# Kernel optimization log

Hardware: AMD Instinct MI355X
Metric: run time of the kernel (lower is better)

## Reference

```python
import jax, jax.numpy as jnp
import numpy as np
from jax import lax

NUM_GROUPS = 256
GROUP_SIZE = 32
RADIUS = 0.1


def setup_inputs() -> dict:
    key = jax.random.key(0)
    k1, k2 = jax.random.split(key)
    B, N, C = 8, 16384, 128
    # xyz in unit cube so radius=0.1 ball query is meaningful
    p = jax.random.uniform(k1, (B, N, 3), dtype=jnp.float32)
    x = jax.random.normal(k2, (B, C, N), dtype=jnp.float32)
    return {"p": p, "x": x}


def furthest_point_sample(p, m):
    # p: [B,N,3] -> idx [B,m]; standard FPS starting at index 0
    B, N, _ = p.shape

    def step(carry, _):
        dist, last = carry
        cur = jnp.take_along_axis(p, last[:, None, None], axis=1)  # [B,1,3]
        d = jnp.sum((p - cur) ** 2, axis=-1)                        # [B,N]
        dist = jnp.minimum(dist, d)
        nxt = jnp.argmax(dist, axis=1).astype(jnp.int32)
        return (dist, nxt), nxt

    dist0 = jnp.full((B, N), 1e10, dtype=p.dtype)
    idx0 = jnp.zeros((B,), dtype=jnp.int32)
    _, rest = lax.scan(step, (dist0, idx0), None, length=m - 1)  # [m-1,B]
    return jnp.concatenate([idx0[:, None], rest.T], axis=1)      # [B,m]


def ball_query(radius, nsample, support, query):
    # support [B,N,3], query [B,M,3] -> idx [B,M,nsample]
    # CUDA ball_query semantics: first `nsample` points (in index order) within
    # radius; slots past the count are padded with the first found index.
    B, N, _ = support.shape
    d2 = jnp.sum((query[:, :, None, :] - support[:, None, :, :]) ** 2, axis=-1)  # [B,M,N]
    within = d2 < radius * radius
    rng = jnp.arange(N, dtype=jnp.int32)
    keys = jnp.where(within, rng, rng + N)   # in-radius first, preserving index order
    neg_vals, _ = lax.top_k(-keys, nsample)  # nsample smallest keys
    keys_k = -neg_vals                       # [B,M,nsample], ascending
    idx = keys_k % N
    valid = keys_k < N
    return jnp.where(valid, idx, idx[..., :1])  # pad with first neighbor (center itself)


def reference(p, x):
    B, C, N = x.shape
    idx = furthest_point_sample(p, NUM_GROUPS)                              # [B,M] int32
    center_p = jnp.take_along_axis(p, idx[:, :, None].astype(jnp.int32), axis=1)  # [B,M,3]
    center_x = jnp.take_along_axis(x, idx[:, None, :], axis=2)[..., None]   # [B,C,M,1]

    nidx = ball_query(RADIUS, GROUP_SIZE, p, center_p)                      # [B,M,ns]
    bidx = jnp.arange(B)[:, None, None]
    gp = p[bidx, nidx]                                                      # [B,M,ns,3]
    # relative xyz (QueryAndGroup relative_xyz=True, normalize_dp=False)
    grouped_p = gp.transpose(0, 3, 1, 2) - center_p.transpose(0, 2, 1)[:, :, :, None]  # [B,3,M,ns]
    fj = x.transpose(0, 2, 1)[bidx, nidx].transpose(0, 3, 1, 2)             # [B,C,M,ns]
    return grouped_p, center_p, fj, center_x
```

## Files before the change

### kernel.cpp

```cpp
#include <hip/hip_runtime.h>
#include <hip/hip_bf16.h>

#define BB 8
#define NN 16384
#define CC 128
#define MM 256
#define NS 32
#define FPS_T 1024
#define PPT (NN / FPS_T)

#define OFF_GP  0
#define OFF_CP  196608
#define OFF_FJ  202752
#define OFF_CX  8591360

__global__ __launch_bounds__(FPS_T)
__attribute__((amdgpu_waves_per_eu(4, 4)))
void fps_kernel(const float* __restrict__ p, int* __restrict__ idx_out)
{
    __shared__ float s_xy[NN * 2];
    __shared__ unsigned long long s_key[2][16];

    const int b = blockIdx.x;
    const int t = threadIdx.x;
    const int lane = t & 63;
    const float* pb = p + (size_t)b * NN * 3;

    float pz[PPT], dist[PPT];
#pragma unroll
    for (int k = 0; k < PPT; ++k) {
        const int n = t + k * FPS_T;
        s_xy[2 * n + 0] = pb[n * 3 + 0];
        s_xy[2 * n + 1] = pb[n * 3 + 1];
        pz[k] = pb[n * 3 + 2];
        dist[k] = 1e10f;
    }
#pragma unroll
    for (int k = 0; k < PPT; ++k) {
        asm volatile("" : "+v"(pz[k]));
    }

    float cx = pb[0], cy = pb[1], cz = pb[2];
    if (t == 0) idx_out[b * MM + 0] = 0;
    __syncthreads();

    for (int i = 1; i < MM; ++i) {
        float bv = -1.0f;
#pragma unroll
        for (int k = 0; k < PPT; ++k) {
            const int n = t + k * FPS_T;
            const float2 xy = *(const float2*)&s_xy[2 * n];
            const float dx = __fsub_rn(xy.x, cx);
            const float dy = __fsub_rn(xy.y, cy);
            const float dz = __fsub_rn(pz[k], cz);
            const float d = __fadd_rn(
                __fadd_rn(__fmul_rn(dx, dx), __fmul_rn(dy, dy)),
                __fmul_rn(dz, dz));
            const float nd = fminf(dist[k], d);
            dist[k] = nd;
            bv = fmaxf(bv, nd);
        }
        int kb = 0;
#pragma unroll
        for (int k = PPT - 1; k >= 0; --k) {
            if (dist[k] == bv) kb = k;
        }
        const int bn = t + (kb << 10);
        unsigned long long key =
            ((unsigned long long)__float_as_uint(bv) << 32) |
            (unsigned int)(~bn);
#pragma unroll
        for (int off = 32; off > 0; off >>= 1) {
            const unsigned long long ok = __shfl_xor(key, off);
            if (ok > key) key = ok;
        }
        const int buf = i & 1;
        if (lane == 0) s_key[buf][t >> 6] = key;
        __syncthreads();
        unsigned long long fk = s_key[buf][lane & 15];
#pragma unroll
        for (int off = 8; off > 0; off >>= 1) {
            const unsigned long long ok = __shfl_xor(fk, off);
            if (ok > fk) fk = ok;
        }
        const int fn = __builtin_amdgcn_readfirstlane(~((unsigned int)fk));
        cx = pb[fn * 3 + 0];
        cy = pb[fn * 3 + 1];
        cz = pb[fn * 3 + 2];
        if (t == 0) idx_out[b * MM + i] = fn;
    }
}

__global__ __launch_bounds__(64) void ballq_kernel(
    const float* __restrict__ p, const int* __restrict__ idx,
    int* __restrict__ nidx, float* __restrict__ grouped_p,
    float* __restrict__ center_p)
{
    const int bm = blockIdx.x;
    const int b = bm >> 8;
    const int m = bm & 255;
    const int lane = threadIdx.x;
    const float* pb = p + (size_t)b * NN * 3;

    const int cidx = idx[bm];
    const float cx = pb[cidx * 3 + 0];
    const float cy = pb[cidx * 3 + 1];
    const float cz = pb[cidx * 3 + 2];

    if (lane < 3) {
        center_p[bm * 3 + lane] = (lane == 0) ? cx : (lane == 1) ? cy : cz;
    }

    const float R2 = 0.01f;

    __shared__ int lidx[NS];

    int found = 0;
    for (int base = 0; base < NN && found < NS; base += 128) {
        const int n0 = base + lane;
        const int n1 = base + 64 + lane;
        const float dx0 = __fsub_rn(pb[n0 * 3 + 0], cx);
        const float dy0 = __fsub_rn(pb[n0 * 3 + 1], cy);
        const float dz0 = __fsub_rn(pb[n0 * 3 + 2], cz);
        const float d20 = __fadd_rn(
            __fadd_rn(__fmul_rn(dx0, dx0), __fmul_rn(dy0, dy0)),
            __fmul_rn(dz0, dz0));
        const float dx1 = __fsub_rn(pb[n1 * 3 + 0], cx);
        const float dy1 = __fsub_rn(pb[n1 * 3 + 1], cy);
        const float dz1 = __fsub_rn(pb[n1 * 3 + 2], cz);
        const float d21 = __fadd_rn(
            __fadd_rn(__fmul_rn(dx1, dx1), __fmul_rn(dy1, dy1)),
            __fmul_rn(dz1, dz1));
        const bool w0 = d20 < R2;
        const bool w1 = d21 < R2;
        const unsigned long long m0 = __ballot(w0);
        const unsigned long long m1 = __ballot(w1);
        const int pc0 = (int)__popcll(m0);
        const unsigned long long below = (1ull << lane) - 1ull;
        const int slot0 = found + __popcll(m0 & below);
        const int slot1 = found + pc0 + __popcll(m1 & below);
        if (w0 && slot0 < NS) lidx[slot0] = n0;
        if (w1 && slot1 < NS) lidx[slot1] = n1;
        found += pc0 + (int)__popcll(m1);
    }
    __syncthreads();

    const int nfound = found < NS ? found : NS;
    if (lane < NS) {
        const int s = lane;
        const int n = (s < nfound) ? lidx[s] : lidx[0];
        nidx[bm * NS + s] = n;
        const float gx = __fsub_rn(pb[n * 3 + 0], cx);
        const float gy = __fsub_rn(pb[n * 3 + 1], cy);
        const float gz = __fsub_rn(pb[n * 3 + 2], cz);
        grouped_p[(((size_t)b * 3 + 0) * MM + m) * NS + s] = gx;
        grouped_p[(((size_t)b * 3 + 1) * MM + m) * NS + s] = gy;
        grouped_p[(((size_t)b * 3 + 2) * MM + m) * NS + s] = gz;
    }
}

__global__ __launch_bounds__(256) void fj_kernel(
    const float* __restrict__ x, const int* __restrict__ nidx,
    float* __restrict__ fj)
{
    const int bm = blockIdx.x;
    const int b = bm >> 8;
    const int m = bm & 255;

    __shared__ int lidx[NS];
    if (threadIdx.x < NS) lidx[threadIdx.x] = nidx[bm * NS + threadIdx.x];
    __syncthreads();

    const int s  = threadIdx.x & 31;
    const int c0 = threadIdx.x >> 5;
    const int n = lidx[s];
    const float* xb = x + (size_t)b * CC * NN;
    float* ob = fj + (size_t)b * CC * MM * NS + (size_t)m * NS + s;

#pragma unroll
    for (int c = c0; c < CC; c += 8) {
        ob[(size_t)c * MM * NS] = xb[(size_t)c * NN + n];
    }
}

__global__ __launch_bounds__(256) void cx_kernel(
    const float* __restrict__ x, const int* __restrict__ idx,
    float* __restrict__ center_x)
{
    const int bc = blockIdx.x;
    const int b = bc >> 7;
    const int m = threadIdx.x;
    const int n = idx[b * MM + m];
    center_x[(size_t)bc * MM + m] = x[(size_t)bc * NN + n];
}

extern "C" void kernel_launch(void* const* d_in, const int* in_sizes, int n_in,
                              void* d_out, int out_size, void* d_ws, size_t ws_size,
                              hipStream_t stream) {
    const float* p = (const float*)d_in[0];
    const float* x = (const float*)d_in[1];
    float* out = (float*)d_out;

    float* grouped_p = out + OFF_GP;
    float* center_p  = out + OFF_CP;
    float* fj        = out + OFF_FJ;
    float* center_x  = out + OFF_CX;

    int* idx  = (int*)d_ws;
    int* nidx = idx + BB * MM;

    fps_kernel<<<BB, FPS_T, 0, stream>>>(p, idx);
    ballq_kernel<<<BB * MM, 64, 0, stream>>>(p, idx, nidx, grouped_p, center_p);
    fj_kernel<<<BB * MM, 256, 0, stream>>>(x, nidx, fj);
    cx_kernel<<<BB * CC, 256, 0, stream>>>(x, idx, center_x);
}
```

Measured before the change: 686.5 us.

## Split FPS across four blocks per batch with global-memory slot synchronization

Furthest point sampling is spread over 4 workgroups per batch (32 blocks instead of 8), each owning a quarter of the points. Per-iteration argmax keys are exchanged through zeroed global slots with agent-scope atomics and spin-waiting, which replaces the block-level __syncthreads reduction. This cuts the per-iteration distance work per block and uses more CUs, at the cost of a global-memory round trip each iteration. The slot buffer borrows the fj output region, which fj_kernel overwrites later. It relies on all 32 blocks being resident at once, and the spin has a bounded retry count.

Result: slower. 2.664 ms (+288.0%).

```diff
diff --git a/kernel.cpp b/kernel.cpp
--- a/kernel.cpp
+++ b/kernel.cpp
@@ -6,32 +6,47 @@
 #define CC 128
 #define MM 256
 #define NS 32
-#define FPS_T 1024
-#define PPT (NN / FPS_T)
+
+#define NB 4
+#define FT 512
+#define NPB (NN / NB)
+#define PPT (NPB / FT)
+#define WPB 8
+#define SLOTS_PER_ITER (NB * WPB)
+#define SYNC_U64 (BB * MM * SLOTS_PER_ITER)
 
 #define OFF_GP  0
 #define OFF_CP  196608
 #define OFF_FJ  202752
 #define OFF_CX  8591360
 
-__global__ __launch_bounds__(FPS_T)
-__attribute__((amdgpu_waves_per_eu(4, 4)))
-void fps_kernel(const float* __restrict__ p, int* __restrict__ idx_out)
-{
-    __shared__ float s_xy[NN * 2];
-    __shared__ unsigned long long s_key[2][16];
-
-    const int b = blockIdx.x;
-    const int t = threadIdx.x;
+__global__ __launch_bounds__(1024) void zero_kernel(unsigned long long* sync)
+{
+    sync[blockIdx.x * 1024 + threadIdx.x] = 0ull;
+}
+
+__global__ __launch_bounds__(FT) void fps_kernel(
+    const float* __restrict__ p, int* __restrict__ idx_out,
+    unsigned long long* __restrict__ sync)
+{
+    __shared__ float s_xy[NPB * 2];
+
+    const int gb   = blockIdx.x;
+    const int r    = gb >> 2;
+    const int blk  = gb & (NB - 1);
+    const int t    = threadIdx.x;
     const int lane = t & 63;
-    const float* pb = p + (size_t)b * NN * 3;
+    const int w    = t >> 6;
+    const float* pb = p + (size_t)r * NN * 3;
+    const int base = blk * NPB;
 
     float pz[PPT], dist[PPT];
 #pragma unroll
     for (int k = 0; k < PPT; ++k) {
-        const int n = t + k * FPS_T;
-        s_xy[2 * n + 0] = pb[n * 3 + 0];
-        s_xy[2 * n + 1] = pb[n * 3 + 1];
+        const int nl = t + k * FT;
+        const int n  = base + nl;
+        s_xy[2 * nl + 0] = pb[n * 3 + 0];
+        s_xy[2 * nl + 1] = pb[n * 3 + 1];
         pz[k] = pb[n * 3 + 2];
         dist[k] = 1e10f;
     }
@@ -41,15 +56,17 @@
     }
 
     float cx = pb[0], cy = pb[1], cz = pb[2];
-    if (t == 0) idx_out[b * MM + 0] = 0;
+    if (blk == 0 && t == 0) idx_out[r * MM + 0] = 0;
     __syncthreads();
+
+    unsigned long long* slots_b = sync + (size_t)r * MM * SLOTS_PER_ITER;
+    const int myslot = blk * WPB + w;
 
     for (int i = 1; i < MM; ++i) {
         float bv = -1.0f;
 #pragma unroll
         for (int k = 0; k < PPT; ++k) {
-            const int n = t + k * FPS_T;
-            const float2 xy = *(const float2*)&s_xy[2 * n];
+            const float2 xy = *(const float2*)&s_xy[2 * (t + k * FT)];
             const float dx = __fsub_rn(xy.x, cx);
             const float dy = __fsub_rn(xy.y, cy);
             const float dz = __fsub_rn(pz[k], cz);
@@ -65,7 +82,7 @@
         for (int k = PPT - 1; k >= 0; --k) {
             if (dist[k] == bv) kb = k;
         }
-        const int bn = t + (kb << 10);
+        const int bn = base + t + kb * FT;
         unsigned long long key =
             ((unsigned long long)__float_as_uint(bv) << 32) |
             (unsigned int)(~bn);
@@ -74,20 +91,28 @@
             const unsigned long long ok = __shfl_xor(key, off);
             if (ok > key) key = ok;
         }
-        const int buf = i & 1;
-        if (lane == 0) s_key[buf][t >> 6] = key;
-        __syncthreads();
-        unsigned long long fk = s_key[buf][lane & 15];
-#pragma unroll
-        for (int off = 8; off > 0; off >>= 1) {
-            const unsigned long long ok = __shfl_xor(fk, off);
-            if (ok > fk) fk = ok;
-        }
-        const int fn = __builtin_amdgcn_readfirstlane(~((unsigned int)fk));
-        cx = pb[fn * 3 + 0];
-        cy = pb[fn * 3 + 1];
-        cz = pb[fn * 3 + 2];
-        if (t == 0) idx_out[b * MM + i] = fn;
+        unsigned long long* it_slots = slots_b + (size_t)i * SLOTS_PER_ITER;
+        if (lane == 0) {
+            __hip_atomic_store(&it_slots[myslot], key, __ATOMIC_RELEASE,
+                               __HIP_MEMORY_SCOPE_AGENT);
+        }
+        unsigned long long my;
+        int tries = 0;
+        do {
+            my = __hip_atomic_load(&it_slots[lane & 31], __ATOMIC_ACQUIRE,
+                                   __HIP_MEMORY_SCOPE_AGENT);
+        } while (!__all(my != 0ull) && ++tries < 65536);
+#pragma unroll
+        for (int off = 16; off > 0; off >>= 1) {
+            const unsigned long long ok = __shfl_xor(my, off);
+            if (ok > my) my = ok;
+        }
+        const int fn = ~((unsigned int)my);
+        if (blk == 0 && t == 0) idx_out[r * MM + i] = fn;
+        const int fnu = __builtin_amdgcn_readfirstlane(fn);
+        cx = pb[fnu * 3 + 0];
+        cy = pb[fnu * 3 + 1];
+        cz = pb[fnu * 3 + 2];
     }
 }
 
@@ -209,7 +234,10 @@
     int* idx  = (int*)d_ws;
     int* nidx = idx + BB * MM;
 
-    fps_kernel<<<BB, FPS_T, 0, stream>>>(p, idx);
+    unsigned long long* sync = (unsigned long long*)(out + OFF_FJ);
+
+    zero_kernel<<<SYNC_U64 / 1024, 1024, 0, stream>>>(sync);
+    fps_kernel<<<BB * NB, FT, 0, stream>>>(p, idx, sync);
     ballq_kernel<<<BB * MM, 64, 0, stream>>>(p, idx, nidx, grouped_p, center_p);
     fj_kernel<<<BB * MM, 256, 0, stream>>>(x, nidx, fj);
     cx_kernel<<<BB * CC, 256, 0, stream>>>(x, idx, center_x);
```
